# Performance work log

Hardware: AMD Instinct MI355X
Metric: run time of the kernel (lower is better)

The kernel has to match this reference:

```python
import jax, jax.numpy as jnp
import numpy as np

N_USERS = 100000
N_ITEMS = 50000
N_EDGES = 2000000
D = 64
EPS = 1e-12  # F.normalize default eps


def setup_inputs() -> dict:
    key = jax.random.key(0)
    k1, k2, k3, k4 = jax.random.split(key, 4)
    x = jax.random.normal(k1, (N_USERS + N_ITEMS, D), dtype=jnp.float32)
    beta = jax.random.normal(k2, (N_USERS,), dtype=jnp.float32) * 0.1
    u = jax.random.randint(k3, (N_EDGES,), 0, N_USERS)
    i = jax.random.randint(k4, (N_EDGES,), 0, N_ITEMS)
    ones = jnp.ones((N_EDGES,), jnp.float32)
    # degree vectors (clamped to >=1 so sqrt-normalization is well-defined)
    du = jnp.maximum(jax.ops.segment_sum(ones, u, num_segments=N_USERS), 1.0)
    di = jnp.maximum(jax.ops.segment_sum(ones, i, num_segments=N_ITEMS), 1.0)
    return {"x": x, "beta": beta, "du": du, "di": di, "u": u, "i": i}


def reference(x, beta, du, di, u, i):
    # split into user/item blocks
    xu, xi = x[:N_USERS], x[N_USERS:]
    # row-wise L2 normalize (torch F.normalize)
    z = x / jnp.maximum(jnp.linalg.norm(x, axis=1, keepdims=True), EPS)
    zu, zi = z[:N_USERS], z[N_USERS:]
    # per-edge score and omega weight: 4/((1+e^-s)(1+e^s)) == 4*sig(s)*(1-sig(s))
    s = jnp.sum(zu[u] * zi[i], axis=1) - beta[u]          # [E]
    sig = jax.nn.sigmoid(s)
    w = 4.0 * sig * (1.0 - sig)
    w = w / jnp.sqrt(du[u]) / jnp.sqrt(di[i])             # degree normalization
    w = w[:, None]                                        # [E,1]
    # scatter-add aggregation back to users and items
    dxu = jax.ops.segment_sum(w * xi[i], u, num_segments=N_USERS)  # [n,D]
    dxi = jax.ops.segment_sum(w * xu[u], i, num_segments=N_ITEMS)  # [m,D]
    return jnp.concatenate([dxu, dxi], axis=0)
```

## Files before the change

kernel.cpp:

```cpp
#include <hip/hip_runtime.h>
#include <math.h>

#define N_USERS 100000
#define N_ITEMS 50000
#define NR      150000
#define N_EDGES 2000000
#define D       64
#define EPS     1e-12f

#define UPAD 64
#define IPAD 64
#define OVF_CAP 4096

#define NPART 8
#define NSUB  2
#define NCHUNK (NPART * NSUB)
#define UCH (N_USERS / NCHUNK)
#define ICH (N_ITEMS / NCHUNK)
#define FILL_BPP 256
#define FILL_BLOCKS (NPART * FILL_BPP)

#define SCAL_OFF 0u
#define XH_OFF   2400000u
#define CNT_OFF  21600000u
#define UBKT_OFF 22200000u
#define IBKT_OFF 35000000u
#define OVFC_OFF 47800000u
#define OVF_OFF  47800004u
#define WS_A4    47816388u

#define C_SCAL 0u
#define C_HEAD 2400000u
#define C_NXTU 3000000u
#define C_NXTI 11000000u
#define WS_C   19000000u

__device__ __forceinline__ unsigned short f2bf(float v) {
    unsigned int b = __float_as_uint(v);
    b += 0x7FFFu + ((b >> 16) & 1u);
    return (unsigned short)(b >> 16);
}
#define BF_LO(w) __uint_as_float((w) << 16)
#define BF_HI(w) __uint_as_float((w) & 0xFFFF0000u)

__global__ void prep_kernel(const float* __restrict__ x,
                            const float* __restrict__ beta,
                            const float* __restrict__ du,
                            const float* __restrict__ di,
                            float4* __restrict__ scal,
                            unsigned short* __restrict__ xh) {
    int gid  = blockIdx.x * blockDim.x + threadIdx.x;
    int r    = gid >> 6;
    int lane = gid & 63;
    if (r >= NR) return;

    float v = x[r * D + lane];
    xh[r * D + lane] = f2bf(v);

    float ss = v * v;
    #pragma unroll
    for (int m = 32; m >= 1; m >>= 1) ss += __shfl_xor(ss, m);

    if (lane == 0) {
        float invn = 1.0f / fmaxf(sqrtf(ss), EPS);
        float deg  = (r < N_USERS) ? du[r] : di[r - N_USERS];
        float b    = (r < N_USERS) ? beta[r] : 0.0f;
        scal[r] = make_float4(invn, rsqrtf(deg), b, 0.0f);
    }
}

__global__ void fillx_kernel(const int* __restrict__ u,
                             const int* __restrict__ i,
                             int* __restrict__ cnt,
                             unsigned short* __restrict__ ubkt,
                             unsigned int* __restrict__ ibkt,
                             int* __restrict__ ovfc,
                             int* __restrict__ ovf) {
    int p   = blockIdx.x & (NPART - 1);
    int qb  = blockIdx.x >> 3;
    int tid = qb * blockDim.x + threadIdx.x;
    const int stride = FILL_BPP * 256;

    #pragma unroll
    for (int sub = 0; sub < NSUB; ++sub) {
        int c   = p * NSUB + sub;
        int ulo = c * UCH, uhi = ulo + UCH;
        int ilo = c * ICH, ihi = ilo + ICH;

        for (int e = tid; e < N_EDGES; e += stride) {
            int uu = __builtin_nontemporal_load(u + e);
            int ii = __builtin_nontemporal_load(i + e);

            if (uu >= ulo && uu < uhi) {
                int s = atomicAdd(&cnt[uu], 1);
                if (s < UPAD) {
                    ubkt[(size_t)uu * UPAD + s] = (unsigned short)ii;
                } else {
                    int pp = atomicAdd(ovfc, 1);
                    if (pp < OVF_CAP) ovf[pp] = (e << 1);
                }
            }
            if (ii >= ilo && ii < ihi) {
                int s = atomicAdd(&cnt[N_USERS + ii], 1);
                if (s < IPAD) {
                    ibkt[(size_t)ii * IPAD + s] = (unsigned int)uu;
                } else {
                    int pp = atomicAdd(ovfc, 1);
                    if (pp < OVF_CAP) ovf[pp] = (e << 1) | 1;
                }
            }
        }
    }
}

__global__ void gatherA_kernel(const unsigned short* __restrict__ xh,
                               const float4* __restrict__ scal,
                               const int* __restrict__ cnt,
                               const unsigned short* __restrict__ ubkt,
                               const unsigned int* __restrict__ ibkt,
                               float* __restrict__ out) {
    int gid  = blockIdx.x * blockDim.x + threadIdx.x;
    int r    = gid >> 6;
    int lane = gid & 63;
    if (r >= NR) return;

    int g = lane >> 3;
    int q = lane & 7;

    float4 sc = scal[r];
    uint4 hs = *(const uint4*)(xh + (size_t)r * D + q * 8);
    float xs0 = BF_LO(hs.x), xs1 = BF_HI(hs.x);
    float xs2 = BF_LO(hs.y), xs3 = BF_HI(hs.y);
    float xs4 = BF_LO(hs.z), xs5 = BF_HI(hs.z);
    float xs6 = BF_LO(hs.w), xs7 = BF_HI(hs.w);

    float a0=0.f,a1=0.f,a2=0.f,a3=0.f,a4=0.f,a5=0.f,a6=0.f,a7=0.f;

    if (r < N_USERS) {
        int deg = cnt[r];
        if (deg > UPAD) deg = UPAD;
        int iters = (deg + 7) >> 3;

        for (int it = 0; it < iters; ++it) {
            int idx = it * 8 + g;
            bool valid = (idx < deg);
            int nb = N_USERS + (int)ubkt[(size_t)r * UPAD + (valid ? idx : 0)];

            float4 so = scal[nb];
            uint4 ho = *(const uint4*)(xh + (size_t)nb * D + q * 8);
            float o0 = BF_LO(ho.x), o1 = BF_HI(ho.x);
            float o2 = BF_LO(ho.y), o3 = BF_HI(ho.y);
            float o4 = BF_LO(ho.z), o5 = BF_HI(ho.z);
            float o6 = BF_LO(ho.w), o7 = BF_HI(ho.w);

            float p = xs0*o0 + xs1*o1 + xs2*o2 + xs3*o3
                    + xs4*o4 + xs5*o5 + xs6*o6 + xs7*o7;
            p += __shfl_xor(p, 1);
            p += __shfl_xor(p, 2);
            p += __shfl_xor(p, 4);

            float sv  = p * sc.x * so.x - sc.z;
            float sig = 1.0f / (1.0f + __expf(-sv));
            float w   = 4.0f * sig * (1.0f - sig) * sc.y * so.y;
            w = valid ? w : 0.0f;

            a0 = fmaf(w, o0, a0); a1 = fmaf(w, o1, a1);
            a2 = fmaf(w, o2, a2); a3 = fmaf(w, o3, a3);
            a4 = fmaf(w, o4, a4); a5 = fmaf(w, o5, a5);
            a6 = fmaf(w, o6, a6); a7 = fmaf(w, o7, a7);
        }
    } else {
        int ri = r - N_USERS;
        int deg = cnt[r];
        if (deg > IPAD) deg = IPAD;
        int iters = (deg + 7) >> 3;

        for (int it = 0; it < iters; ++it) {
            int idx = it * 8 + g;
            bool valid = (idx < deg);
            int nb = (int)ibkt[(size_t)ri * IPAD + (valid ? idx : 0)];

            float4 so = scal[nb];
            uint4 ho = *(const uint4*)(xh + (size_t)nb * D + q * 8);
            float o0 = BF_LO(ho.x), o1 = BF_HI(ho.x);
            float o2 = BF_LO(ho.y), o3 = BF_HI(ho.y);
            float o4 = BF_LO(ho.z), o5 = BF_HI(ho.z);
            float o6 = BF_LO(ho.w), o7 = BF_HI(ho.w);

            float p = xs0*o0 + xs1*o1 + xs2*o2 + xs3*o3
                    + xs4*o4 + xs5*o5 + xs6*o6 + xs7*o7;
            p += __shfl_xor(p, 1);
            p += __shfl_xor(p, 2);
            p += __shfl_xor(p, 4);

            float sv  = p * sc.x * so.x - so.z;
            float sig = 1.0f / (1.0f + __expf(-sv));
            float w   = 4.0f * sig * (1.0f - sig) * sc.y * so.y;
            w = valid ? w : 0.0f;

            a0 = fmaf(w, o0, a0); a1 = fmaf(w, o1, a1);
            a2 = fmaf(w, o2, a2); a3 = fmaf(w, o3, a3);
            a4 = fmaf(w, o4, a4); a5 = fmaf(w, o5, a5);
            a6 = fmaf(w, o6, a6); a7 = fmaf(w, o7, a7);
        }
    }

    #pragma unroll
    for (int m = 8; m <= 32; m <<= 1) {
        a0 += __shfl_xor(a0, m); a1 += __shfl_xor(a1, m);
        a2 += __shfl_xor(a2, m); a3 += __shfl_xor(a3, m);
        a4 += __shfl_xor(a4, m); a5 += __shfl_xor(a5, m);
        a6 += __shfl_xor(a6, m); a7 += __shfl_xor(a7, m);
    }

    if (g == 0) {
        float4* o4p = (float4*)(out + (size_t)r * D + q * 8);
        o4p[0] = make_float4(a0, a1, a2, a3);
        o4p[1] = make_float4(a4, a5, a6, a7);
    }
}

__global__ void ovf_kernel(const float* __restrict__ x,
                           const float4* __restrict__ scal,
                           const int* __restrict__ u,
                           const int* __restrict__ i,
                           const int* __restrict__ ovfc,
                           const int* __restrict__ ovf,
                           float* __restrict__ out) {
    int n = *ovfc;
    if (n > OVF_CAP) n = OVF_CAP;
    int gid  = blockIdx.x * blockDim.x + threadIdx.x;
    int wave = gid >> 6;
    int lane = gid & 63;
    int nw   = (gridDim.x * blockDim.x) >> 6;

    for (int k = wave; k < n; k += nw) {
        int pk = ovf[k];
        int e = pk >> 1, side = pk & 1;
        int uu = u[e];
        int ir = N_USERS + i[e];
        float xu = x[uu * D + lane];
        float xi = x[ir * D + lane];
        float p = xu * xi;
        #pragma unroll
        for (int m = 32; m >= 1; m >>= 1) p += __shfl_xor(p, m);
        float4 su = scal[uu];
        float4 si = scal[ir];
        float sv  = p * su.x * si.x - su.z;
        float sig = 1.0f / (1.0f + __expf(-sv));
        float w   = 4.0f * sig * (1.0f - sig) * su.y * si.y;
        if (side == 0) atomicAdd(&out[(size_t)uu * D + lane], w * xi);
        else           atomicAdd(&out[(size_t)ir * D + lane], w * xu);
    }
}

__global__ void scal_kernel(const float* __restrict__ x,
                            const float* __restrict__ beta,
                            const float* __restrict__ du,
                            const float* __restrict__ di,
                            float4* __restrict__ scal) {
    int gid  = blockIdx.x * blockDim.x + threadIdx.x;
    int r    = gid >> 6;
    int lane = gid & 63;
    if (r >= NR) return;
    float v  = x[r * D + lane];
    float ss = v * v;
    #pragma unroll
    for (int m = 32; m >= 1; m >>= 1) ss += __shfl_xor(ss, m);
    if (lane == 0) {
        float invn = 1.0f / fmaxf(sqrtf(ss), EPS);
        float deg  = (r < N_USERS) ? du[r] : di[r - N_USERS];
        float b    = (r < N_USERS) ? beta[r] : 0.0f;
        scal[r] = make_float4(invn, rsqrtf(deg), b, 0.0f);
    }
}

__global__ void link_kernel(const int* __restrict__ u,
                            const int* __restrict__ i,
                            int* __restrict__ head,
                            int* __restrict__ next_u,
                            int* __restrict__ next_i) {
    int e = blockIdx.x * blockDim.x + threadIdx.x;
    if (e >= N_EDGES) return;
    int uu = u[e];
    int ii = N_USERS + i[e];
    next_u[e] = atomicExch(&head[uu], e);
    next_i[e] = atomicExch(&head[ii], e);
}

__global__ void gather_kernel(const float4* __restrict__ x4,
                              const float4* __restrict__ scal,
                              const int* __restrict__ head,
                              const int* __restrict__ next_u,
                              const int* __restrict__ next_i,
                              const int* __restrict__ u,
                              const int* __restrict__ i,
                              float4* __restrict__ out4) {
    int gid  = blockIdx.x * blockDim.x + threadIdx.x;
    int r    = gid >> 6;
    int lane = gid & 63;
    if (r >= NR) return;
    int g = lane >> 4;
    int q = lane & 15;
    bool isu = (r < N_USERS);
    const int* __restrict__ nxt = isu ? next_u : next_i;
    const int* __restrict__ oid = isu ? i : u;
    int obase = isu ? N_USERS : 0;
    float4 sc = scal[r];
    float4 xs = x4[r * 16 + q];
    float4 acc = make_float4(0.f, 0.f, 0.f, 0.f);
    int e  = head[r];
    int c0 = e; { int t = nxt[(c0 >= 0) ? c0 : 0]; e = (c0 >= 0) ? t : -1; }
    int c1 = e; { int t = nxt[(c1 >= 0) ? c1 : 0]; e = (c1 >= 0) ? t : -1; }
    int c2 = e; { int t = nxt[(c2 >= 0) ? c2 : 0]; e = (c2 >= 0) ? t : -1; }
    int c3 = e; { int t = nxt[(c3 >= 0) ? c3 : 0]; e = (c3 >= 0) ? t : -1; }
    while (c0 >= 0) {
        int n0 = e; { int t = nxt[(n0 >= 0) ? n0 : 0]; e = (n0 >= 0) ? t : -1; }
        int n1 = e; { int t = nxt[(n1 >= 0) ? n1 : 0]; e = (n1 >= 0) ? t : -1; }
        int n2 = e; { int t = nxt[(n2 >= 0) ? n2 : 0]; e = (n2 >= 0) ? t : -1; }
        int n3 = e; { int t = nxt[(n3 >= 0) ? n3 : 0]; e = (n3 >= 0) ? t : -1; }
        int eg = (g == 0) ? c0 : (g == 1) ? c1 : (g == 2) ? c2 : c3;
        bool valid = (eg >= 0);
        int  es = valid ? eg : c0;
        int  nb = obase + oid[es];
        float4 so = scal[nb];
        float4 xo = x4[nb * 16 + q];
        float p = xs.x * xo.x + xs.y * xo.y + xs.z * xo.z + xs.w * xo.w;
        p += __shfl_xor(p, 1);
        p += __shfl_xor(p, 2);
        p += __shfl_xor(p, 4);
        p += __shfl_xor(p, 8);
        float b   = isu ? sc.z : so.z;
        float sv  = p * sc.x * so.x - b;
        float sig = 1.0f / (1.0f + __expf(-sv));
        float w   = 4.0f * sig * (1.0f - sig) * sc.y * so.y;
        w = valid ? w : 0.0f;
        acc.x = fmaf(w, xo.x, acc.x);
        acc.y = fmaf(w, xo.y, acc.y);
        acc.z = fmaf(w, xo.z, acc.z);
        acc.w = fmaf(w, xo.w, acc.w);
        c0 = n0; c1 = n1; c2 = n2; c3 = n3;
    }
    acc.x += __shfl_xor(acc.x, 16); acc.y += __shfl_xor(acc.y, 16);
    acc.z += __shfl_xor(acc.z, 16); acc.w += __shfl_xor(acc.w, 16);
    acc.x += __shfl_xor(acc.x, 32); acc.y += __shfl_xor(acc.y, 32);
    acc.z += __shfl_xor(acc.z, 32); acc.w += __shfl_xor(acc.w, 32);
    if (g == 0) out4[r * 16 + q] = acc;
}

__global__ void norm_kernel(const float* __restrict__ x,
                            float* __restrict__ invn,
                            int nrows) {
    int gid  = blockIdx.x * blockDim.x + threadIdx.x;
    int wave = gid >> 6;
    int lane = gid & 63;
    if (wave >= nrows) return;
    float v  = x[wave * D + lane];
    float ss = v * v;
    #pragma unroll
    for (int m = 32; m >= 1; m >>= 1) ss += __shfl_xor(ss, m);
    if (lane == 0) invn[wave] = 1.0f / fmaxf(sqrtf(ss), EPS);
}

__global__ void edge_kernel(const float* __restrict__ x,
                            const float* __restrict__ beta,
                            const float* __restrict__ du,
                            const float* __restrict__ di,
                            const int*   __restrict__ u,
                            const int*   __restrict__ i,
                            const float* __restrict__ invn,
                            float* __restrict__ out) {
    int gid  = blockIdx.x * blockDim.x + threadIdx.x;
    int wave = gid >> 6;
    int lane = gid & 63;
    if (wave >= N_EDGES) return;
    int uu = u[wave];
    int ii = i[wave];
    const float xu = x[uu * D + lane];
    const float xi = x[(N_USERS + ii) * D + lane];
    float p = xu * xi;
    #pragma unroll
    for (int m = 32; m >= 1; m >>= 1) p += __shfl_xor(p, m);
    float s   = p * invn[uu] * invn[N_USERS + ii] - beta[uu];
    float sig = 1.0f / (1.0f + __expf(-s));
    float w   = 4.0f * sig * (1.0f - sig) * rsqrtf(du[uu]) * rsqrtf(di[ii]);
    atomicAdd(&out[uu * D + lane],             w * xi);
    atomicAdd(&out[(N_USERS + ii) * D + lane], w * xu);
}

extern "C" void kernel_launch(void* const* d_in, const int* in_sizes, int n_in,
                              void* d_out, int out_size, void* d_ws, size_t ws_size,
                              hipStream_t stream) {
    const float* x    = (const float*)d_in[0];
    const float* beta = (const float*)d_in[1];
    const float* du   = (const float*)d_in[2];
    const float* di   = (const float*)d_in[3];
    const int*   u    = (const int*)d_in[4];
    const int*   i    = (const int*)d_in[5];
    float* out = (float*)d_out;
    char*  ws  = (char*)d_ws;

    if (ws_size >= (size_t)WS_A4) {
        float4*         scal = (float4*)(ws + SCAL_OFF);
        unsigned short* xh   = (unsigned short*)(ws + XH_OFF);
        int*            cnt  = (int*)(ws + CNT_OFF);
        unsigned short* ubkt = (unsigned short*)(ws + UBKT_OFF);
        unsigned int*   ibkt = (unsigned int*)(ws + IBKT_OFF);
        int*            ovfc = (int*)(ws + OVFC_OFF);
        int*            ovf  = (int*)(ws + OVF_OFF);

        hipMemsetAsync(cnt, 0, (size_t)NR * sizeof(int), stream);
        hipMemsetAsync(ovfc, 0, sizeof(int), stream);
        prep_kernel<<<(NR + 3) / 4, 256, 0, stream>>>(x, beta, du, di, scal, xh);
        fillx_kernel<<<FILL_BLOCKS, 256, 0, stream>>>(u, i, cnt, ubkt, ibkt, ovfc, ovf);
        gatherA_kernel<<<(NR + 3) / 4, 256, 0, stream>>>(xh, scal, cnt, ubkt, ibkt, out);
        ovf_kernel<<<64, 256, 0, stream>>>(x, scal, u, i, ovfc, ovf, out);
    } else if (ws_size >= (size_t)WS_C) {
        float4* scal   = (float4*)(ws + C_SCAL);
        int*    head   = (int*)(ws + C_HEAD);
        int*    next_u = (int*)(ws + C_NXTU);
        int*    next_i = (int*)(ws + C_NXTI);

        scal_kernel<<<(NR + 3) / 4, 256, 0, stream>>>(x, beta, du, di, scal);
        hipMemsetAsync(head, 0xFF, (size_t)NR * sizeof(int), stream);
        link_kernel<<<(N_EDGES + 255) / 256, 256, 0, stream>>>(u, i, head, next_u, next_i);
        gather_kernel<<<(NR + 3) / 4, 256, 0, stream>>>((const float4*)x, scal, head,
                                                        next_u, next_i, u, i, (float4*)out);
    } else {
        float* invn = (float*)ws;
        hipMemsetAsync(d_out, 0, (size_t)out_size * sizeof(float), stream);
        norm_kernel<<<(NR + 3) / 4, 256, 0, stream>>>(x, invn, NR);
        edge_kernel<<<(N_EDGES + 3) / 4, 256, 0, stream>>>(x, beta, du, di, u, i, invn, out);
    }
}
```

Measured before the change: 361.4 us.

## Two-pass radix partition of edges before bucket fill to localize atomics

```diff
diff --git a/kernel.cpp b/kernel.cpp
--- a/kernel.cpp
+++ b/kernel.cpp
@@ -8,32 +8,41 @@
 #define D       64
 #define EPS     1e-12f
 
-#define UPAD 64
+#define UPAD 48
 #define IPAD 64
 #define OVF_CAP 4096
 
-#define NPART 8
-#define NSUB  2
-#define NCHUNK (NPART * NSUB)
-#define UCH (N_USERS / NCHUNK)
-#define ICH (N_ITEMS / NCHUNK)
-#define FILL_BPP 256
-#define FILL_BLOCKS (NPART * FILL_BPP)
+#define NCHUNK 8
+#define UCH 12500
+#define ICH 6250
+#define SEGCAP 262144
+
+#define EPT 8
+#define PART_BLOCKS ((N_EDGES + 256*EPT - 1) / (256*EPT))
+#define FILLP_BLOCKS 1024
 
 #define SCAL_OFF 0u
 #define XH_OFF   2400000u
 #define CNT_OFF  21600000u
 #define UBKT_OFF 22200000u
-#define IBKT_OFF 35000000u
-#define OVFC_OFF 47800000u
-#define OVF_OFF  47800004u
-#define WS_A4    47816388u
-
-#define C_SCAL 0u
-#define C_HEAD 2400000u
-#define C_NXTU 3000000u
-#define C_NXTI 11000000u
-#define WS_C   19000000u
+#define IBKT_OFF 31800000u
+#define PART_OFF 44600000u
+#define UCUR_OFF 52988608u
+#define ICUR_OFF 52988640u
+#define OVFC_OFF 52988672u
+#define OVF_OFF  52988680u
+#define WS_P     53021448u
+
+#define A_SCAL 0u
+#define A_XH   2400000u
+#define A_CNT  21600000u
+#define A_UBKT 22200000u
+#define A_IBKT 35000000u
+#define A_OVFC 47800000u
+#define A_OVF  47800008u
+#define WS_A   47832776u
+#define A_UPAD 64
+#define A_IPAD 64
 
 __device__ __forceinline__ unsigned short f2bf(float v) {
     unsigned int b = __float_as_uint(v);
@@ -42,6 +51,12 @@
 }
 #define BF_LO(w) __uint_as_float((w) << 16)
 #define BF_HI(w) __uint_as_float((w) & 0xFFFF0000u)
+
+__global__ void init_kernel(int* ucur, int* icur, int* ovfc) {
+    int t = threadIdx.x;
+    if (t < NCHUNK) { ucur[t] = t * SEGCAP; icur[t] = t * SEGCAP; }
+    if (t == 32) *ovfc = 0;
+}
 
 __global__ void prep_kernel(const float* __restrict__ x,
                             const float* __restrict__ beta,
@@ -69,50 +84,109 @@
     }
 }
 
-__global__ void fillx_kernel(const int* __restrict__ u,
-                             const int* __restrict__ i,
+template<int SIDE>
+__global__ void part_kernel(const int* __restrict__ u,
+                            const int* __restrict__ i,
+                            int* __restrict__ cur,
+                            unsigned int* __restrict__ part,
+                            int* __restrict__ ovfc,
+                            int2* __restrict__ ovf) {
+    __shared__ int h[NCHUNK];
+    __shared__ int base[NCHUNK];
+
+    int tid = threadIdx.x;
+    int e0  = blockIdx.x * (256 * EPT);
+    if (tid < NCHUNK) h[tid] = 0;
+    __syncthreads();
+
+    int bins[EPT];
+    unsigned int vals[EPT];
+    int uus[EPT], iis[EPT];
+
+    #pragma unroll
+    for (int k = 0; k < EPT; ++k) {
+        int e = e0 + k * 256 + tid;
+        bool ok = (e < N_EDGES);
+        int uu = ok ? __builtin_nontemporal_load(u + e) : 0;
+        int ii = ok ? __builtin_nontemporal_load(i + e) : 0;
+        int bin, loc;
+        unsigned int val;
+        if (SIDE == 0) { bin = uu / UCH; loc = uu - bin * UCH;
+                         val = ((unsigned)loc << 16) | (unsigned)ii; }
+        else           { bin = ii / ICH; loc = ii - bin * ICH;
+                         val = ((unsigned)loc << 17) | (unsigned)uu; }
+        bins[k] = ok ? bin : -1;
+        vals[k] = val; uus[k] = uu; iis[k] = ii;
+        if (ok) atomicAdd(&h[bin], 1);
+    }
+    __syncthreads();
+    if (tid < NCHUNK) { base[tid] = atomicAdd(&cur[tid], h[tid]); h[tid] = 0; }
+    __syncthreads();
+
+    #pragma unroll
+    for (int k = 0; k < EPT; ++k) {
+        int b = bins[k];
+        if (b >= 0) {
+            int r   = atomicAdd(&h[b], 1);
+            int off = base[b] + r;
+            if (off < (b + 1) * SEGCAP) {
+                part[off] = vals[k];
+            } else {
+                int pp = atomicAdd(ovfc, 1);
+                if (pp < OVF_CAP) {
+                    int2 rec = (SIDE == 0)
+                      ? make_int2(uus[k], N_USERS + iis[k])
+                      : make_int2(N_USERS + iis[k], uus[k]);
+                    ovf[pp] = rec;
+                }
+            }
+        }
+    }
+}
+
+template<int SIDE>
+__global__ void fillp_kernel(const unsigned int* __restrict__ part,
+                             const int* __restrict__ cur,
                              int* __restrict__ cnt,
                              unsigned short* __restrict__ ubkt,
                              unsigned int* __restrict__ ibkt,
                              int* __restrict__ ovfc,
-                             int* __restrict__ ovf) {
-    int p   = blockIdx.x & (NPART - 1);
-    int qb  = blockIdx.x >> 3;
-    int tid = qb * blockDim.x + threadIdx.x;
-    const int stride = FILL_BPP * 256;
-
-    #pragma unroll
-    for (int sub = 0; sub < NSUB; ++sub) {
-        int c   = p * NSUB + sub;
-        int ulo = c * UCH, uhi = ulo + UCH;
-        int ilo = c * ICH, ihi = ilo + ICH;
-
-        for (int e = tid; e < N_EDGES; e += stride) {
-            int uu = __builtin_nontemporal_load(u + e);
-            int ii = __builtin_nontemporal_load(i + e);
-
-            if (uu >= ulo && uu < uhi) {
-                int s = atomicAdd(&cnt[uu], 1);
-                if (s < UPAD) {
-                    ubkt[(size_t)uu * UPAD + s] = (unsigned short)ii;
-                } else {
-                    int pp = atomicAdd(ovfc, 1);
-                    if (pp < OVF_CAP) ovf[pp] = (e << 1);
-                }
+                             int2* __restrict__ ovf) {
+    int p  = blockIdx.x & (NCHUNK - 1);
+    int jb = blockIdx.x >> 3;
+    int lo = p * SEGCAP;
+    int hi = cur[p];
+    if (hi > (p + 1) * SEGCAP) hi = (p + 1) * SEGCAP;
+
+    for (int k = lo + jb * 256 + (int)threadIdx.x; k < hi; k += 128 * 256) {
+        unsigned int rec = __builtin_nontemporal_load(part + k);
+        if (SIDE == 0) {
+            int loc = rec >> 16;
+            int ii  = rec & 0xFFFF;
+            int uu  = p * UCH + loc;
+            int s = atomicAdd(&cnt[uu], 1);
+            if (s < UPAD) {
+                ubkt[(size_t)uu * UPAD + s] = (unsigned short)ii;
+            } else {
+                int pp = atomicAdd(ovfc, 1);
+                if (pp < OVF_CAP) ovf[pp] = make_int2(uu, N_USERS + ii);
             }
-            if (ii >= ilo && ii < ihi) {
-                int s = atomicAdd(&cnt[N_USERS + ii], 1);
-                if (s < IPAD) {
-                    ibkt[(size_t)ii * IPAD + s] = (unsigned int)uu;
-                } else {
-                    int pp = atomicAdd(ovfc, 1);
-                    if (pp < OVF_CAP) ovf[pp] = (e << 1) | 1;
-                }
+        } else {
+            int loc = rec >> 17;
+            int uu  = rec & 0x1FFFF;
+            int ii  = p * ICH + loc;
+            int s = atomicAdd(&cnt[N_USERS + ii], 1);
+            if (s < IPAD) {
+                ibkt[(size_t)ii * IPAD + s] = (unsigned int)uu;
+            } else {
+                int pp = atomicAdd(ovfc, 1);
+                if (pp < OVF_CAP) ovf[pp] = make_int2(N_USERS + ii, uu);
             }
         }
     }
 }
 
+template<int UP, int IP>
 __global__ void gatherA_kernel(const unsigned short* __restrict__ xh,
                                const float4* __restrict__ scal,
                                const int* __restrict__ cnt,
@@ -138,13 +212,12 @@
 
     if (r < N_USERS) {
         int deg = cnt[r];
-        if (deg > UPAD) deg = UPAD;
+        if (deg > UP) deg = UP;
         int iters = (deg + 7) >> 3;
-
         for (int it = 0; it < iters; ++it) {
             int idx = it * 8 + g;
             bool valid = (idx < deg);
-            int nb = N_USERS + (int)ubkt[(size_t)r * UPAD + (valid ? idx : 0)];
+            int nb = N_USERS + (int)ubkt[(size_t)r * UP + (valid ? idx : 0)];
 
             float4 so = scal[nb];
             uint4 ho = *(const uint4*)(xh + (size_t)nb * D + q * 8);
@@ -172,13 +245,12 @@
     } else {
         int ri = r - N_USERS;
         int deg = cnt[r];
-        if (deg > IPAD) deg = IPAD;
+        if (deg > IP) deg = IP;
         int iters = (deg + 7) >> 3;
-
         for (int it = 0; it < iters; ++it) {
             int idx = it * 8 + g;
             bool valid = (idx < deg);
-            int nb = (int)ibkt[(size_t)ri * IPAD + (valid ? idx : 0)];
+            int nb = (int)ibkt[(size_t)ri * IP + (valid ? idx : 0)];
 
             float4 so = scal[nb];
             uint4 ho = *(const uint4*)(xh + (size_t)nb * D + q * 8);
@@ -220,13 +292,11 @@
     }
 }
 
-__global__ void ovf_kernel(const float* __restrict__ x,
-                           const float4* __restrict__ scal,
-                           const int* __restrict__ u,
-                           const int* __restrict__ i,
-                           const int* __restrict__ ovfc,
-                           const int* __restrict__ ovf,
-                           float* __restrict__ out) {
+__global__ void ovf2_kernel(const float* __restrict__ x,
+                            const float4* __restrict__ scal,
+                            const int* __restrict__ ovfc,
+                            const int2* __restrict__ ovf,
+                            float* __restrict__ out) {
     int n = *ovfc;
     if (n > OVF_CAP) n = OVF_CAP;
     int gid  = blockIdx.x * blockDim.x + threadIdx.x;
@@ -235,125 +305,58 @@
     int nw   = (gridDim.x * blockDim.x) >> 6;
 
     for (int k = wave; k < n; k += nw) {
-        int pk = ovf[k];
-        int e = pk >> 1, side = pk & 1;
-        int uu = u[e];
-        int ir = N_USERS + i[e];
-        float xu = x[uu * D + lane];
-        float xi = x[ir * D + lane];
-        float p = xu * xi;
+        int d  = ovf[k].x;
+        int nb = ovf[k].y;
+        float xd = x[(size_t)d * D + lane];
+        float xn = x[(size_t)nb * D + lane];
+        float p = xd * xn;
         #pragma unroll
         for (int m = 32; m >= 1; m >>= 1) p += __shfl_xor(p, m);
-        float4 su = scal[uu];
-        float4 si = scal[ir];
-        float sv  = p * su.x * si.x - su.z;
+        float4 sd = scal[d];
+        float4 sn = scal[nb];
+        float sv  = p * sd.x * sn.x - (sd.z + sn.z);
         float sig = 1.0f / (1.0f + __expf(-sv));
-        float w   = 4.0f * sig * (1.0f - sig) * su.y * si.y;
-        if (side == 0) atomicAdd(&out[(size_t)uu * D + lane], w * xi);
-        else           atomicAdd(&out[(size_t)ir * D + lane], w * xu);
-    }
-}
-
-__global__ void scal_kernel(const float* __restrict__ x,
-                            const float* __restrict__ beta,
-                            const float* __restrict__ du,
-                            const float* __restrict__ di,
-                            float4* __restrict__ scal) {
+        float w   = 4.0f * sig * (1.0f - sig) * sd.y * sn.y;
+        atomicAdd(&out[(size_t)d * D + lane], w * xn);
+    }
+}
+
+__global__ void fillx_kernel(const int* __restrict__ u,
+                             const int* __restrict__ i,
+                             int* __restrict__ cnt,
+                             unsigned short* __restrict__ ubkt,
+                             unsigned int* __restrict__ ibkt,
+                             int* __restrict__ ovfc,
+                             int2* __restrict__ ovf) {
+    int p   = blockIdx.x & 7;
+    int qb  = blockIdx.x >> 3;
+    int tid = qb * blockDim.x + threadIdx.x;
+    const int stride = 256 * 256;
+    int ulo = p * UCH, uhi = ulo + UCH;
+    int ilo = p * ICH, ihi = ilo + ICH;
+
+    for (int e = tid; e < N_EDGES; e += stride) {
+        int uu = __builtin_nontemporal_load(u + e);
+        int ii = __builtin_nontemporal_load(i + e);
+        if (uu >= ulo && uu < uhi) {
+            int s = atomicAdd(&cnt[uu], 1);
+            if (s < A_UPAD) ubkt[(size_t)uu * A_UPAD + s] = (unsigned short)ii;
+            else { int pp = atomicAdd(ovfc, 1);
+                   if (pp < OVF_CAP) ovf[pp] = make_int2(uu, N_USERS + ii); }
+        }
+        if (ii >= ilo && ii < ihi) {
+            int s = atomicAdd(&cnt[N_USERS + ii], 1);
+            if (s < A_IPAD) ibkt[(size_t)ii * A_IPAD + s] = (unsigned int)uu;
+            else { int pp = atomicAdd(ovfc, 1);
+                   if (pp < OVF_CAP) ovf[pp] = make_int2(N_USERS + ii, uu); }
+        }
+    }
+}
+
+__global__ void norm_kernel(const float* __restrict__ x,
+                            float* __restrict__ invn, int nrows) {
     int gid  = blockIdx.x * blockDim.x + threadIdx.x;
-    int r    = gid >> 6;
-    int lane = gid & 63;
-    if (r >= NR) return;
-    float v  = x[r * D + lane];
-    float ss = v * v;
-    #pragma unroll
-    for (int m = 32; m >= 1; m >>= 1) ss += __shfl_xor(ss, m);
-    if (lane == 0) {
-        float invn = 1.0f / fmaxf(sqrtf(ss), EPS);
-        float deg  = (r < N_USERS) ? du[r] : di[r - N_USERS];
-        float b    = (r < N_USERS) ? beta[r] : 0.0f;
-        scal[r] = make_float4(invn, rsqrtf(deg), b, 0.0f);
-    }
-}
-
-__global__ void link_kernel(const int* __restrict__ u,
-                            const int* __restrict__ i,
-                            int* __restrict__ head,
-                            int* __restrict__ next_u,
-                            int* __restrict__ next_i) {
-    int e = blockIdx.x * blockDim.x + threadIdx.x;
-    if (e >= N_EDGES) return;
-    int uu = u[e];
-    int ii = N_USERS + i[e];
-    next_u[e] = atomicExch(&head[uu], e);
-    next_i[e] = atomicExch(&head[ii], e);
-}
-
-__global__ void gather_kernel(const float4* __restrict__ x4,
-                              const float4* __restrict__ scal,
-                              const int* __restrict__ head,
-                              const int* __restrict__ next_u,
-                              const int* __restrict__ next_i,
-                              const int* __restrict__ u,
-                              const int* __restrict__ i,
-                              float4* __restrict__ out4) {
-    int gid  = blockIdx.x * blockDim.x + threadIdx.x;
-    int r    = gid >> 6;
-    int lane = gid & 63;
-    if (r >= NR) return;
-    int g = lane >> 4;
-    int q = lane & 15;
-    bool isu = (r < N_USERS);
-    const int* __restrict__ nxt = isu ? next_u : next_i;
-    const int* __restrict__ oid = isu ? i : u;
-    int obase = isu ? N_USERS : 0;
-    float4 sc = scal[r];
-    float4 xs = x4[r * 16 + q];
-    float4 acc = make_float4(0.f, 0.f, 0.f, 0.f);
-    int e  = head[r];
-    int c0 = e; { int t = nxt[(c0 >= 0) ? c0 : 0]; e = (c0 >= 0) ? t : -1; }
-    int c1 = e; { int t = nxt[(c1 >= 0) ? c1 : 0]; e = (c1 >= 0) ? t : -1; }
-    int c2 = e; { int t = nxt[(c2 >= 0) ? c2 : 0]; e = (c2 >= 0) ? t : -1; }
-    int c3 = e; { int t = nxt[(c3 >= 0) ? c3 : 0]; e = (c3 >= 0) ? t : -1; }
-    while (c0 >= 0) {
-        int n0 = e; { int t = nxt[(n0 >= 0) ? n0 : 0]; e = (n0 >= 0) ? t : -1; }
-        int n1 = e; { int t = nxt[(n1 >= 0) ? n1 : 0]; e = (n1 >= 0) ? t : -1; }
-        int n2 = e; { int t = nxt[(n2 >= 0) ? n2 : 0]; e = (n2 >= 0) ? t : -1; }
-        int n3 = e; { int t = nxt[(n3 >= 0) ? n3 : 0]; e = (n3 >= 0) ? t : -1; }
-        int eg = (g == 0) ? c0 : (g == 1) ? c1 : (g == 2) ? c2 : c3;
-        bool valid = (eg >= 0);
-        int  es = valid ? eg : c0;
-        int  nb = obase + oid[es];
-        float4 so = scal[nb];
-        float4 xo = x4[nb * 16 + q];
-        float p = xs.x * xo.x + xs.y * xo.y + xs.z * xo.z + xs.w * xo.w;
-        p += __shfl_xor(p, 1);
-        p += __shfl_xor(p, 2);
-        p += __shfl_xor(p, 4);
-        p += __shfl_xor(p, 8);
-        float b   = isu ? sc.z : so.z;
-        float sv  = p * sc.x * so.x - b;
-        float sig = 1.0f / (1.0f + __expf(-sv));
-        float w   = 4.0f * sig * (1.0f - sig) * sc.y * so.y;
-        w = valid ? w : 0.0f;
-        acc.x = fmaf(w, xo.x, acc.x);
-        acc.y = fmaf(w, xo.y, acc.y);
-        acc.z = fmaf(w, xo.z, acc.z);
-        acc.w = fmaf(w, xo.w, acc.w);
-        c0 = n0; c1 = n1; c2 = n2; c3 = n3;
-    }
-    acc.x += __shfl_xor(acc.x, 16); acc.y += __shfl_xor(acc.y, 16);
-    acc.z += __shfl_xor(acc.z, 16); acc.w += __shfl_xor(acc.w, 16);
-    acc.x += __shfl_xor(acc.x, 32); acc.y += __shfl_xor(acc.y, 32);
-    acc.z += __shfl_xor(acc.z, 32); acc.w += __shfl_xor(acc.w, 32);
-    if (g == 0) out4[r * 16 + q] = acc;
-}
-
-__global__ void norm_kernel(const float* __restrict__ x,
-                            float* __restrict__ invn,
-                            int nrows) {
-    int gid  = blockIdx.x * blockDim.x + threadIdx.x;
-    int wave = gid >> 6;
-    int lane = gid & 63;
+    int wave = gid >> 6, lane = gid & 63;
     if (wave >= nrows) return;
     float v  = x[wave * D + lane];
     float ss = v * v;
@@ -366,18 +369,16 @@
                             const float* __restrict__ beta,
                             const float* __restrict__ du,
                             const float* __restrict__ di,
-                            const int*   __restrict__ u,
-                            const int*   __restrict__ i,
+                            const int* __restrict__ u,
+                            const int* __restrict__ i,
                             const float* __restrict__ invn,
                             float* __restrict__ out) {
     int gid  = blockIdx.x * blockDim.x + threadIdx.x;
-    int wave = gid >> 6;
-    int lane = gid & 63;
+    int wave = gid >> 6, lane = gid & 63;
     if (wave >= N_EDGES) return;
-    int uu = u[wave];
-    int ii = i[wave];
-    const float xu = x[uu * D + lane];
-    const float xi = x[(N_USERS + ii) * D + lane];
+    int uu = u[wave], ii = i[wave];
+    float xu = x[uu * D + lane];
+    float xi = x[(N_USERS + ii) * D + lane];
     float p = xu * xi;
     #pragma unroll
     for (int m = 32; m >= 1; m >>= 1) p += __shfl_xor(p, m);
@@ -400,32 +401,46 @@
     float* out = (float*)d_out;
     char*  ws  = (char*)d_ws;
 
-    if (ws_size >= (size_t)WS_A4) {
+    if (ws_size >= (size_t)WS_P) {
         float4*         scal = (float4*)(ws + SCAL_OFF);
         unsigned short* xh   = (unsigned short*)(ws + XH_OFF);
         int*            cnt  = (int*)(ws + CNT_OFF);
         unsigned short* ubkt = (unsigned short*)(ws + UBKT_OFF);
         unsigned int*   ibkt = (unsigned int*)(ws + IBKT_OFF);
+        unsigned int*   part = (unsigned int*)(ws + PART_OFF);
+        int*            ucur = (int*)(ws + UCUR_OFF);
+        int*            icur = (int*)(ws + ICUR_OFF);
         int*            ovfc = (int*)(ws + OVFC_OFF);
-        int*            ovf  = (int*)(ws + OVF_OFF);
+        int2*           ovf  = (int2*)(ws + OVF_OFF);
+
+        hipMemsetAsync(cnt, 0, (size_t)NR * sizeof(int), stream);
+        init_kernel<<<1, 64, 0, stream>>>(ucur, icur, ovfc);
+        prep_kernel<<<(NR + 3) / 4, 256, 0, stream>>>(x, beta, du, di, scal, xh);
+
+        part_kernel<0><<<PART_BLOCKS, 256, 0, stream>>>(u, i, ucur, part, ovfc, ovf);
+        fillp_kernel<0><<<FILLP_BLOCKS, 256, 0, stream>>>(part, ucur, cnt, ubkt, ibkt, ovfc, ovf);
+        part_kernel<1><<<PART_BLOCKS, 256, 0, stream>>>(u, i, icur, part, ovfc, ovf);
+        fillp_kernel<1><<<FILLP_BLOCKS, 256, 0, stream>>>(part, icur, cnt, ubkt, ibkt, ovfc, ovf);
+
+        gatherA_kernel<UPAD, IPAD><<<(NR + 3) / 4, 256, 0, stream>>>(
+            xh, scal, cnt, ubkt, ibkt, out);
+        ovf2_kernel<<<64, 256, 0, stream>>>(x, scal, ovfc, ovf, out);
+    } else if (ws_size >= (size_t)WS_A) {
+        float4*         scal = (float4*)(ws + A_SCAL);
+        unsigned short* xh   = (unsigned short*)(ws + A_XH);
+        int*            cnt  = (int*)(ws + A_CNT);
+        unsigned short* ubkt = (unsigned short*)(ws + A_UBKT);
+        unsigned int*   ibkt = (unsigned int*)(ws + A_IBKT);
+        int*            ovfc = (int*)(ws + A_OVFC);
+        int2*           ovf  = (int2*)(ws + A_OVF);
 
         hipMemsetAsync(cnt, 0, (size_t)NR * sizeof(int), stream);
         hipMemsetAsync(ovfc, 0, sizeof(int), stream);
         prep_kernel<<<(NR + 3) / 4, 256, 0, stream>>>(x, beta, du, di, scal, xh);
-        fillx_kernel<<<FILL_BLOCKS, 256, 0, stream>>>(u, i, cnt, ubkt, ibkt, ovfc, ovf);
-        gatherA_kernel<<<(NR + 3) / 4, 256, 0, stream>>>(xh, scal, cnt, ubkt, ibkt, out);
-        ovf_kernel<<<64, 256, 0, stream>>>(x, scal, u, i, ovfc, ovf, out);
-    } else if (ws_size >= (size_t)WS_C) {
-        float4* scal   = (float4*)(ws + C_SCAL);
-        int*    head   = (int*)(ws + C_HEAD);
-        int*    next_u = (int*)(ws + C_NXTU);
-        int*    next_i = (int*)(ws + C_NXTI);
-
-        scal_kernel<<<(NR + 3) / 4, 256, 0, stream>>>(x, beta, du, di, scal);
-        hipMemsetAsync(head, 0xFF, (size_t)NR * sizeof(int), stream);
-        link_kernel<<<(N_EDGES + 255) / 256, 256, 0, stream>>>(u, i, head, next_u, next_i);
-        gather_kernel<<<(NR + 3) / 4, 256, 0, stream>>>((const float4*)x, scal, head,
-                                                        next_u, next_i, u, i, (float4*)out);
+        fillx_kernel<<<2048, 256, 0, stream>>>(u, i, cnt, ubkt, ibkt, ovfc, ovf);
+        gatherA_kernel<A_UPAD, A_IPAD><<<(NR + 3) / 4, 256, 0, stream>>>(
+            xh, scal, cnt, ubkt, ibkt, out);
+        ovf2_kernel<<<64, 256, 0, stream>>>(x, scal, ovfc, ovf, out);
     } else {
         float* invn = (float*)ws;
         hipMemsetAsync(d_out, 0, (size_t)out_size * sizeof(float), stream);
```

Result: faster. 348.3 us (-3.6%).
